# Optimization experiments

Measured on AMD Instinct MI355X. Metric: run time of the kernel, lower is better.

The kernel has to match this reference:

```python
import jax, jax.numpy as jnp
import numpy as np

D_MODEL = 2048
NUM_HEADS = 16
D_KV = D_MODEL // NUM_HEADS
THETA = 10000.0


def apply_rope(x, pos):
    # x: [B, H, S, d_kv], pos: [S] int
    d = x.shape[-1]
    inv_freq = 1.0 / (THETA ** (jnp.arange(0, d, 2, dtype=jnp.float32) / d))  # [d/2]
    ang = pos.astype(jnp.float32)[:, None] * inv_freq[None, :]  # [S, d/2]
    cos, sin = jnp.cos(ang), jnp.sin(ang)  # broadcast over B,H
    x1 = x[..., 0::2]
    x2 = x[..., 1::2]
    r1 = x1 * cos - x2 * sin
    r2 = x1 * sin + x2 * cos
    return jnp.stack([r1, r2], axis=-1).reshape(x.shape)


def setup_inputs() -> dict:
    key = jax.random.key(0)
    k = jax.random.split(key, 5)
    B, S = 2, 2048
    x = jax.random.normal(k[0], (B, S, D_MODEL), dtype=jnp.float32)
    scale = 1.0 / np.sqrt(D_MODEL)
    Wq = jax.random.normal(k[1], (D_MODEL, D_MODEL), dtype=jnp.float32) * scale
    Wk = jax.random.normal(k[2], (D_MODEL, D_MODEL), dtype=jnp.float32) * scale
    Wv = jax.random.normal(k[3], (D_MODEL, D_MODEL), dtype=jnp.float32) * scale
    Wo = jax.random.normal(k[4], (D_MODEL, D_MODEL), dtype=jnp.float32) * scale
    token_position = jnp.arange(S, dtype=jnp.int64 if jax.config.jax_enable_x64 else jnp.int32)
    return {"x": x, "Wq": Wq, "Wk": Wk, "Wv": Wv, "Wo": Wo, "token_position": token_position}


def reference(x, Wq, Wk, Wv, Wo, token_position):
    B, S, _ = x.shape
    def heads(y):
        return y.reshape(B, S, NUM_HEADS, D_KV).transpose(0, 2, 1, 3)  # [B,H,S,d]
    Q = heads(jnp.einsum('bsd,df->bsf', x, Wq))
    K = heads(jnp.einsum('bsd,df->bsf', x, Wk))
    V = heads(jnp.einsum('bsd,df->bsf', x, Wv))
    Q = apply_rope(Q, token_position)
    K = apply_rope(K, token_position)
    scale = 1.0 / jnp.sqrt(jnp.asarray(D_KV, dtype=x.dtype))
    scores = jnp.einsum('bhqd,bhkd->bhqk', Q, K) * scale  # [B,H,S,S]
    causal = jnp.tril(jnp.ones((S, S), dtype=bool))
    scores = jnp.where(causal, scores, -jnp.inf)
    attn = jax.nn.softmax(scores, axis=-1)
    out = jnp.einsum('bhqk,bhkd->bhqd', attn, V)  # [B,H,S,d]
    out = out.transpose(0, 2, 1, 3).reshape(B, S, D_MODEL)
    return jnp.einsum('bsd,df->bsf', out, Wo)
```

## Files before the change

kernel.cpp:

```cpp
#include <hip/hip_runtime.h>
#include <hip/hip_bf16.h>

#define S 2048
#define DM 2048
#define NH 16
#define DH 128

typedef __attribute__((ext_vector_type(8))) short short8;
typedef __attribute__((ext_vector_type(4))) float floatx4;
typedef unsigned short u16;
typedef unsigned int u32;

__device__ __forceinline__ u16 f2bf(float f) {
  union { float f; u32 u; } v; v.f = f;
  u32 r = v.u + 0x7fffu + ((v.u >> 16) & 1u);
  return (u16)(r >> 16);
}
__device__ __forceinline__ u32 pack2(float lo, float hi) {
  float2 f; f.x = lo; f.y = hi;
  __hip_bfloat162 h = __float22bfloat162_rn(f);
  union { __hip_bfloat162 h; u32 u; } c; c.h = h;
  return c.u;
}

__device__ __forceinline__ floatx4 mfma16(short8 a, short8 b, floatx4 c) {
  return __builtin_amdgcn_mfma_f32_16x16x32_bf16(a, b, c, 0, 0, 0);
}

__device__ __forceinline__ void async_cp16(const u16* g, u16* l) {
  __builtin_amdgcn_global_load_lds(
      (const __attribute__((address_space(1))) void*)g,
      (__attribute__((address_space(3))) void*)l, 16, 0, 0);
}

__global__ void conv_x_k(const float* __restrict__ x, u16* __restrict__ xb) {
  int gid = blockIdx.x * 256 + threadIdx.x;
  float4 v = ((const float4*)x)[gid];
  uint2 p; p.x = pack2(v.x, v.y); p.y = pack2(v.z, v.w);
  ((uint2*)xb)[gid] = p;
}

__global__ void conv_w_k(const float* __restrict__ W0, const float* __restrict__ W1,
                         const float* __restrict__ W2, const float* __restrict__ W3,
                         u16* __restrict__ out) {
  __shared__ float tile[32][33];
  const float* W = blockIdx.z == 0 ? W0 : blockIdx.z == 1 ? W1 : blockIdx.z == 2 ? W2 : W3;
  u16* O = out + (size_t)blockIdx.z * DM * DM;
  int tx = threadIdx.x & 31, ty = threadIdx.x >> 5;
  int k0 = blockIdx.y * 32, n0 = blockIdx.x * 32;
#pragma unroll
  for (int j = 0; j < 4; j++)
    tile[ty + j * 8][tx] = W[(size_t)(k0 + ty + j * 8) * DM + n0 + tx];
  __syncthreads();
#pragma unroll
  for (int j = 0; j < 4; j++)
    O[(size_t)(n0 + ty + j * 8) * DM + k0 + tx] = f2bf(tile[tx][ty + j * 8]);
}

#define BM 256
#define BN 128
#define BK 32
#define NT 64

#define BARRIER __builtin_amdgcn_s_barrier()
#define SB __builtin_amdgcn_sched_barrier(0)
#define LGKM0 asm volatile("s_waitcnt lgkmcnt(0)" ::: "memory")

#define STG_A(q, j, koff) \
  async_cp16(pAg + (size_t)(j) * 64 * DM + (koff), &As[q][soff + (j) * 2048])
#define STG_B(q, j, koff) \
  async_cp16(pBg + (size_t)(j) * 64 * DM + (koff), &Bs[q][soff + (j) * 2048])

#define PH0(p) { \
    a0 = *(const short8*)&As[p][arow + xk]; \
    a1 = *(const short8*)&As[p][arow + 512 + xk]; \
    a2 = *(const short8*)&As[p][arow + 1024 + xk]; \
    a3 = *(const short8*)&As[p][arow + 1536 + xk]; \
    a4 = *(const short8*)&As[p][arow + 2048 + xk]; \
    a5 = *(const short8*)&As[p][arow + 2560 + xk]; \
    a6 = *(const short8*)&As[p][arow + 3072 + xk]; \
    a7 = *(const short8*)&As[p][arow + 3584 + xk]; \
    b0 = *(const short8*)&Bs[p][brow + xk]; \
    b1 = *(const short8*)&Bs[p][brow + 512 + xk]; \
    b2 = *(const short8*)&Bs[p][brow + 1024 + xk]; \
    b3 = *(const short8*)&Bs[p][brow + 1536 + xk]; \
    BARRIER; LGKM0; SB; \
    __builtin_amdgcn_s_setprio(1); \
    acc[0][0] = mfma16(a0, b0, acc[0][0]); \
    acc[1][0] = mfma16(a1, b0, acc[1][0]); \
    acc[2][0] = mfma16(a2, b0, acc[2][0]); \
    acc[3][0] = mfma16(a3, b0, acc[3][0]); \
    acc[0][1] = mfma16(a0, b1, acc[0][1]); \
    acc[1][1] = mfma16(a1, b1, acc[1][1]); \
    acc[2][1] = mfma16(a2, b1, acc[2][1]); \
    acc[3][1] = mfma16(a3, b1, acc[3][1]); \
    acc[0][2] = mfma16(a0, b2, acc[0][2]); \
    acc[1][2] = mfma16(a1, b2, acc[1][2]); \
    acc[2][2] = mfma16(a2, b2, acc[2][2]); \
    acc[3][2] = mfma16(a3, b2, acc[3][2]); \
    acc[0][3] = mfma16(a0, b3, acc[0][3]); \
    acc[1][3] = mfma16(a1, b3, acc[1][3]); \
    acc[2][3] = mfma16(a2, b3, acc[2][3]); \
    acc[3][3] = mfma16(a3, b3, acc[3][3]); \
    __builtin_amdgcn_s_setprio(0); \
    BARRIER; }

#define PH1(p, koff2, PRE2, LAST) { \
    if (PRE2) { STG_B(p, 0, koff2); STG_B(p, 1, koff2); \
                STG_A(p, 0, koff2); STG_A(p, 1, koff2); \
                STG_A(p, 2, koff2); STG_A(p, 3, koff2); } \
    SB; \
    __builtin_amdgcn_s_setprio(1); \
    acc[4][0] = mfma16(a4, b0, acc[4][0]); \
    acc[5][0] = mfma16(a5, b0, acc[5][0]); \
    acc[6][0] = mfma16(a6, b0, acc[6][0]); \
    acc[7][0] = mfma16(a7, b0, acc[7][0]); \
    acc[4][1] = mfma16(a4, b1, acc[4][1]); \
    acc[5][1] = mfma16(a5, b1, acc[5][1]); \
    acc[6][1] = mfma16(a6, b1, acc[6][1]); \
    acc[7][1] = mfma16(a7, b1, acc[7][1]); \
    acc[4][2] = mfma16(a4, b2, acc[4][2]); \
    acc[5][2] = mfma16(a5, b2, acc[5][2]); \
    acc[6][2] = mfma16(a6, b2, acc[6][2]); \
    acc[7][2] = mfma16(a7, b2, acc[7][2]); \
    acc[4][3] = mfma16(a4, b3, acc[4][3]); \
    acc[5][3] = mfma16(a5, b3, acc[5][3]); \
    acc[6][3] = mfma16(a6, b3, acc[6][3]); \
    acc[7][3] = mfma16(a7, b3, acc[7][3]); \
    __builtin_amdgcn_s_setprio(0); SB; \
    if (!LAST) { \
      if (PRE2) { asm volatile("s_waitcnt vmcnt(6)" ::: "memory"); } \
      else      { asm volatile("s_waitcnt vmcnt(0)" ::: "memory"); } \
      BARRIER; SB; } }

__global__ __launch_bounds__(256, 2)
void gemm_k(const u16* __restrict__ A, const u16* __restrict__ Wt,
            u16* __restrict__ oQ, u16* __restrict__ oK, u16* __restrict__ oV,
            const int* __restrict__ tp)
{
  __shared__ u16 As[2][BM * BK];
  __shared__ u16 Bs[2][BN * BK];
  const int t = threadIdx.x;
  const int w = t >> 6, lane = t & 63;
  const int l16 = lane & 15, quad = lane >> 4;
  const int wr = w >> 1, wc = w & 1;
  const int m0 = blockIdx.y * BM, n0 = blockIdx.x * BN;
  const u16* Bt = Wt + (size_t)blockIdx.z * DM * DM;

  const int srow = t >> 2;
  const int sc = ((t & 3) ^ ((t >> 3) & 3)) * 8;
  const u16* pAg = A + (size_t)(m0 + srow) * DM + sc;
  const u16* pBg = Bt + (size_t)(n0 + srow) * DM + sc;
  const int soff = t * 8;

  const int arow = (wr * 128 + l16) * 32;
  const int brow = (wc * 64 + l16) * 32;
  const int xk = ((quad ^ ((l16 >> 1) & 3)) << 3);

  floatx4 acc[8][4] = {};
  short8 a0, a1, a2, a3, a4, a5, a6, a7, b0, b1, b2, b3;

  STG_B(0, 0, 0); STG_B(0, 1, 0);
  STG_A(0, 0, 0); STG_A(0, 1, 0); STG_A(0, 2, 0); STG_A(0, 3, 0);
  STG_B(1, 0, BK); STG_B(1, 1, BK);
  STG_A(1, 0, BK); STG_A(1, 1, BK); STG_A(1, 2, BK); STG_A(1, 3, BK);
  SB;
  asm volatile("s_waitcnt vmcnt(6)" ::: "memory");
  BARRIER; SB;

  for (int it = 0; it < 31; ++it) {
    const int kE = (2 * it + 2) * BK;
    const int kO = (2 * it + 3) * BK;
    PH0(0) PH1(0, kE, 1, 0)
    PH0(1) PH1(1, kO, 1, 0)
  }
  PH0(0) PH1(0, 0, 0, 0)
  PH0(1) PH1(1, 0, 0, 1)

  const int mwb = m0 + wr * 128;
  const int nwb = n0 + wc * 64;
  if ((int)blockIdx.z == 2) {
#pragma unroll
    for (int mi = 0; mi < 8; mi++) {
      int m = mwb + mi * 16 + quad * 4;
      int b = m >> 11, s = m & (S - 1);
#pragma unroll
      for (int ni = 0; ni < 4; ni++) {
        int f = nwb + ni * 16 + l16;
        int h = f >> 7, dh = f & (DH - 1);
        uint2 pk; pk.x = pack2(acc[mi][ni][0], acc[mi][ni][1]);
        pk.y = pack2(acc[mi][ni][2], acc[mi][ni][3]);
        *(uint2*)&oV[((size_t)(b * NH + h) * DH + dh) * S + s] = pk;
      }
    }
  } else {
    u16* Out = ((int)blockIdx.z == 0) ? oQ : oK;
    const float qs = ((int)blockIdx.z == 0) ? 0.12752780f : 1.0f;
#pragma unroll
    for (int mi = 0; mi < 8; mi++) {
#pragma unroll
      for (int r = 0; r < 4; r++) {
        int m = mwb + mi * 16 + quad * 4 + r;
        int b = m >> 11, s = m & (S - 1);
        int ps = tp[s];
#pragma unroll
        for (int ni = 0; ni < 4; ni++) {
          int f = nwb + ni * 16 + l16;
          int h = f >> 7, dh = f & (DH - 1);
          float own = acc[mi][ni][r];
          float oth = __shfl_xor(own, 1, 64);
          float fr = __expf((float)(dh & ~1) * (-9.210340371976184f / 128.0f));
          float ang = (float)ps * fr;
          float sn, cs; __sincosf(ang, &sn, &cs);
          float res = (dh & 1) ? (oth * sn + own * cs) : (own * cs - oth * sn);
          Out[((size_t)(b * NH + h) * S + s) * DH + dh] = f2bf(res * qs);
        }
      }
    }
  }
}

__global__ __launch_bounds__(256, 4)
void oproj_k(const u16* __restrict__ A, const u16* __restrict__ Wt,
             float* __restrict__ oO)
{
  __shared__ u16 As2[128 * 32];
  __shared__ u16 Bs2[128 * 32];
  const int t = threadIdx.x;
  const int w = t >> 6, lane = t & 63;
  const int l16 = lane & 15, quad = lane >> 4;
  const int m0 = blockIdx.y * 128, n0 = blockIdx.x * 128;
  const int wm = (w >> 1) * 64, wn = (w & 1) * 64;
  const u16* Bt = Wt + (size_t)3 * DM * DM;

  const u16* pA[2]; const u16* pB[2]; u16* lA[2]; u16* lB[2];
#pragma unroll
  for (int i = 0; i < 2; i++) {
    int unit = i * 256 + t;
    int row = unit >> 2, s = unit & 3;
    int c = s ^ ((row >> 1) & 3);
    pA[i] = A + (size_t)(m0 + row) * DM + c * 8;
    pB[i] = Bt + (size_t)(n0 + row) * DM + c * 8;
    lA[i] = &As2[unit * 8];
    lB[i] = &Bs2[unit * 8];
  }

  floatx4 acc[4][4] = {};

  for (int k0 = 0; k0 < DM; k0 += 32) {
#pragma unroll
    for (int i = 0; i < 2; i++) {
      async_cp16(pA[i] + k0, lA[i]);
      async_cp16(pB[i] + k0, lB[i]);
    }
    __syncthreads();
    short8 af[4], bfr[4];
#pragma unroll
    for (int i = 0; i < 4; i++) {
      int row = wm + i * 16 + l16;
      af[i] = *(short8*)&As2[(row * 4 + (quad ^ ((row >> 1) & 3))) * 8];
    }
#pragma unroll
    for (int i = 0; i < 4; i++) {
      int row = wn + i * 16 + l16;
      bfr[i] = *(short8*)&Bs2[(row * 4 + (quad ^ ((row >> 1) & 3))) * 8];
    }
#pragma unroll
    for (int mi = 0; mi < 4; mi++)
#pragma unroll
      for (int ni = 0; ni < 4; ni++)
        acc[mi][ni] = mfma16(af[mi], bfr[ni], acc[mi][ni]);
    __syncthreads();
  }

#pragma unroll
  for (int mi = 0; mi < 4; mi++) {
    int m = m0 + wm + mi * 16 + quad * 4;
#pragma unroll
    for (int ni = 0; ni < 4; ni++) {
      int n = n0 + wn + ni * 16 + l16;
#pragma unroll
      for (int r = 0; r < 4; r++)
        oO[(size_t)(m + r) * DM + n] = acc[mi][ni][r];
    }
  }
}

#define ATILE(p, i) { \
    const int k0a = (i) * 64; \
    floatx4 sc[4] = {}; \
    __builtin_amdgcn_s_setprio(1); \
    _Pragma("unroll") \
    for (int hh = 0; hh < 4; hh++) { \
      int row = hh * 16 + l16; \
      _Pragma("unroll") \
      for (int kc = 0; kc < 4; kc++) { \
        short8 kf = *(short8*)&Ks[p][row * 128 + (((kc * 4 + quad) ^ l16) << 3)]; \
        sc[hh] = mfma16(kf, aq[kc], sc[hh]); \
      } \
    } \
    __builtin_amdgcn_s_setprio(0); \
    if (k0a + 64 > qt) { \
      _Pragma("unroll") \
      for (int hh = 0; hh < 4; hh++) \
        _Pragma("unroll") \
        for (int r = 0; r < 4; r++) { \
          int j = k0a + hh * 16 + quad * 4 + r; \
          if (j > qt + l16) sc[hh][r] = -3.0e38f; \
        } \
    } \
    _Pragma("unroll") \
    for (int hh = 0; hh < 4; hh++) { \
      float e0 = __builtin_amdgcn_exp2f(fminf(sc[hh][0], 44.0f)); \
      float e1 = __builtin_amdgcn_exp2f(fminf(sc[hh][1], 44.0f)); \
      float e2 = __builtin_amdgcn_exp2f(fminf(sc[hh][2], 44.0f)); \
      float e3 = __builtin_amdgcn_exp2f(fminf(sc[hh][3], 44.0f)); \
      lsum += (e0 + e1) + (e2 + e3); \
      uint2 pk; pk.x = pack2(e0, e1); pk.y = pack2(e2, e3); \
      int su = (2 * hh + (quad >> 1)) ^ pxor; \
      *(uint2*)&Pw[l16 * 64 + su * 8 + (quad & 1) * 4] = pk; \
    } \
    LGKM0; SB; \
    BARRIER;                        \
    if ((i) + 2 < nt) { \
      _Pragma("unroll") \
      for (int j = 0; j < 4; j++) \
        async_cp16(pK[j] + (size_t)(k0a + 128) * DH, &Ks[p][lKo[j]]); \
    } \
    __builtin_amdgcn_s_setprio(1); \
    _Pragma("unroll") \
    for (int c = 0; c < 2; c++) { \
      short8 pf = *(short8*)&Pw[l16 * 64 + (((4 * c + quad) ^ pxor) << 3)]; \
      _Pragma("unroll") \
      for (int t8 = 0; t8 < 8; t8++) { \
        int row = t8 * 16 + l16; \
        short8 av = *(short8*)&Vs[p][row * 64 + (((c * 4 + quad) ^ (l16 & 7)) << 3)]; \
        o[t8] = mfma16(av, pf, o[t8]); \
      } \
    } \
    __builtin_amdgcn_s_setprio(0); \
    LGKM0; SB; \
    BARRIER;                        \
    if ((i) + 2 < nt) { \
      _Pragma("unroll") \
      for (int j = 0; j < 4; j++) \
        async_cp16(pV[j] + k0a + 128, &Vs[p][lVo[j]]); \
    } \
    if ((i) + 1 < nt) { \
      SB; \
      if ((i) + 2 < nt) { asm volatile("s_waitcnt vmcnt(8)" ::: "memory"); } \
      else              { asm volatile("s_waitcnt vmcnt(0)" ::: "memory"); } \
      BARRIER; SB; \
    } \
  }

__global__ __launch_bounds__(256, 2)
void attn_k(const u16* __restrict__ Q, const u16* __restrict__ K,
            const u16* __restrict__ Vt, u16* __restrict__ O)
{
  __shared__ u16 Ks[2][64 * 128];
  __shared__ u16 Vs[2][128 * 64];
  __shared__ u16 P[4][16 * 64];
  const int t = threadIdx.x, w = t >> 6, lane = t & 63;
  const int l16 = lane & 15, quad = lane >> 4;
  const int task = blockIdx.x;
  const int bh = task & 31, b = bh >> 4, h = bh & 15;
  const int g = 31 - (task >> 5);
  const int qg = g * 64;
  const int qt = qg + w * 16;
  const int nt = g + 1;
  const u16* Qb = Q + (size_t)bh * S * DH;
  const u16* Kb = K + (size_t)bh * S * DH;
  const u16* Vb = Vt + (size_t)bh * DH * S;
  u16* Pw = P[w];
  const int pxor = l16 & 7;

  const u16* pK[4]; int lKo[4];
  const u16* pV[4]; int lVo[4];
#pragma unroll
  for (int j = 0; j < 4; j++) {
    int kr = w * 16 + j * 4 + quad;
    int ks = l16;
    int kc = ks ^ (kr & 15);
    pK[j] = Kb + (size_t)kr * DH + kc * 8;
    lKo[j] = kr * 128 + ks * 8;
    int vr = w * 32 + j * 8 + (lane >> 3);
    int vs = lane & 7;
    int vc = vs ^ (vr & 7);
    pV[j] = Vb + (size_t)vr * S + vc * 8;
    lVo[j] = vr * 64 + vs * 8;
  }

  short8 aq[4];
#pragma unroll
  for (int kc = 0; kc < 4; kc++)
    aq[kc] = *(const short8*)&Qb[(size_t)(qt + l16) * DH + kc * 32 + quad * 8];

  floatx4 o[8] = {};
  float lsum = 0.0f;

#pragma unroll
  for (int j = 0; j < 4; j++) async_cp16(pK[j], &Ks[0][lKo[j]]);
#pragma unroll
  for (int j = 0; j < 4; j++) async_cp16(pV[j], &Vs[0][lVo[j]]);
  if (nt > 1) {
#pragma unroll
    for (int j = 0; j < 4; j++) async_cp16(pK[j] + (size_t)64 * DH, &Ks[1][lKo[j]]);
#pragma unroll
    for (int j = 0; j < 4; j++) async_cp16(pV[j] + 64, &Vs[1][lVo[j]]);
    SB;
    asm volatile("s_waitcnt vmcnt(8)" ::: "memory");
  } else {
    SB;
    asm volatile("s_waitcnt vmcnt(0)" ::: "memory");
  }
  BARRIER; SB;

  int i = 0;
  for (; i + 2 <= nt; i += 2) {
    ATILE(0, i)
    ATILE(1, i + 1)
  }
  if (i < nt) { ATILE(0, i) }

  float l = lsum + __shfl_xor(lsum, 16, 64);
  l += __shfl_xor(l, 32, 64);
  float inv = __builtin_amdgcn_rcpf(l);
#pragma unroll
  for (int t8 = 0; t8 < 8; t8++) {
    uint2 pa;
    pa.x = pack2(o[t8][0] * inv, o[t8][1] * inv);
    pa.y = pack2(o[t8][2] * inv, o[t8][3] * inv);
    *(uint2*)&O[((size_t)(b * S + qt + l16)) * DM + h * DH + t8 * 16 + quad * 4] = pa;
  }
}

extern "C" void kernel_launch(void* const* d_in, const int* in_sizes, int n_in,
                              void* d_out, int out_size, void* d_ws, size_t ws_size,
                              hipStream_t stream) {
  const float* x  = (const float*)d_in[0];
  const float* Wq = (const float*)d_in[1];
  const float* Wk = (const float*)d_in[2];
  const float* Wv = (const float*)d_in[3];
  const float* Wo = (const float*)d_in[4];
  const int*   tp = (const int*)d_in[5];

  char* ws = (char*)d_ws;
  u16* Wt = (u16*)ws;
  u16* xb = (u16*)(ws + 33554432);
  u16* Qb = (u16*)(ws + 50331648);
  u16* Kb = (u16*)(ws + 67108864);
  u16* Vb = (u16*)(ws + 83886080);
  u16* Ob = (u16*)(ws + 100663296);

  conv_x_k<<<8192, 256, 0, stream>>>(x, xb);
  conv_w_k<<<dim3(64, 64, 4), 256, 0, stream>>>(Wq, Wk, Wv, Wo, Wt);
  gemm_k<<<dim3(16, 16, 3), 256, 0, stream>>>(xb, Wt, Qb, Kb, Vb, tp);
  attn_k<<<1024, 256, 0, stream>>>(Qb, Kb, Vb, Ob);
  oproj_k<<<dim3(16, 32), 256, 0, stream>>>(Ob, Wt, (float*)d_out);
}
```

Measured before the change: 369.3 us.

## Double attention query tile per block to 128 rows, halving K/V loads

```diff
diff --git a/kernel.cpp b/kernel.cpp
--- a/kernel.cpp
+++ b/kernel.cpp
@@ -288,37 +288,44 @@
 
 #define ATILE(p, i) { \
     const int k0a = (i) * 64; \
-    floatx4 sc[4] = {}; \
-    __builtin_amdgcn_s_setprio(1); \
-    _Pragma("unroll") \
-    for (int hh = 0; hh < 4; hh++) { \
-      int row = hh * 16 + l16; \
+    if (k0a <= qt + 31) { \
       _Pragma("unroll") \
-      for (int kc = 0; kc < 4; kc++) { \
-        short8 kf = *(short8*)&Ks[p][row * 128 + (((kc * 4 + quad) ^ l16) << 3)]; \
-        sc[hh] = mfma16(kf, aq[kc], sc[hh]); \
+      for (int hh = 0; hh < 4; hh++) { \
+        int row = hh * 16 + l16; \
+        floatx4 s0 = {0.f, 0.f, 0.f, 0.f}; \
+        floatx4 s1 = {0.f, 0.f, 0.f, 0.f}; \
+        __builtin_amdgcn_s_setprio(1); \
+        _Pragma("unroll") \
+        for (int kc = 0; kc < 4; kc++) { \
+          short8 kf = *(short8*)&Ks[p][row * 128 + (((kc * 4 + quad) ^ l16) << 3)]; \
+          s0 = mfma16(kf, aq0[kc], s0); \
+          s1 = mfma16(kf, aq1[kc], s1); \
+        } \
+        __builtin_amdgcn_s_setprio(0); \
+        if (k0a + 64 > qt) { \
+          _Pragma("unroll") \
+          for (int r = 0; r < 4; r++) { \
+            int jj = k0a + hh * 16 + quad * 4 + r; \
+            if (jj > qt + l16) s0[r] = -3.0e38f; \
+            if (jj > qt + 16 + l16) s1[r] = -3.0e38f; \
+          } \
+        } \
+        int su = (2 * hh + (quad >> 1)) ^ pxor; \
+        float e0 = __builtin_amdgcn_exp2f(fminf(s0[0], 44.0f)); \
+        float e1 = __builtin_amdgcn_exp2f(fminf(s0[1], 44.0f)); \
+        float e2 = __builtin_amdgcn_exp2f(fminf(s0[2], 44.0f)); \
+        float e3 = __builtin_amdgcn_exp2f(fminf(s0[3], 44.0f)); \
+        lsum0 += (e0 + e1) + (e2 + e3); \
+        uint2 pk0; pk0.x = pack2(e0, e1); pk0.y = pack2(e2, e3); \
+        *(uint2*)&Pw[l16 * 64 + su * 8 + (quad & 1) * 4] = pk0; \
+        e0 = __builtin_amdgcn_exp2f(fminf(s1[0], 44.0f)); \
+        e1 = __builtin_amdgcn_exp2f(fminf(s1[1], 44.0f)); \
+        e2 = __builtin_amdgcn_exp2f(fminf(s1[2], 44.0f)); \
+        e3 = __builtin_amdgcn_exp2f(fminf(s1[3], 44.0f)); \
+        lsum1 += (e0 + e1) + (e2 + e3); \
+        uint2 pk1; pk1.x = pack2(e0, e1); pk1.y = pack2(e2, e3); \
+        *(uint2*)&Pw[(16 + l16) * 64 + su * 8 + (quad & 1) * 4] = pk1; \
       } \
-    } \
-    __builtin_amdgcn_s_setprio(0); \
-    if (k0a + 64 > qt) { \
-      _Pragma("unroll") \
-      for (int hh = 0; hh < 4; hh++) \
-        _Pragma("unroll") \
-        for (int r = 0; r < 4; r++) { \
-          int j = k0a + hh * 16 + quad * 4 + r; \
-          if (j > qt + l16) sc[hh][r] = -3.0e38f; \
-        } \
-    } \
-    _Pragma("unroll") \
-    for (int hh = 0; hh < 4; hh++) { \
-      float e0 = __builtin_amdgcn_exp2f(fminf(sc[hh][0], 44.0f)); \
-      float e1 = __builtin_amdgcn_exp2f(fminf(sc[hh][1], 44.0f)); \
-      float e2 = __builtin_amdgcn_exp2f(fminf(sc[hh][2], 44.0f)); \
-      float e3 = __builtin_amdgcn_exp2f(fminf(sc[hh][3], 44.0f)); \
-      lsum += (e0 + e1) + (e2 + e3); \
-      uint2 pk; pk.x = pack2(e0, e1); pk.y = pack2(e2, e3); \
-      int su = (2 * hh + (quad >> 1)) ^ pxor; \
-      *(uint2*)&Pw[l16 * 64 + su * 8 + (quad & 1) * 4] = pk; \
     } \
     LGKM0; SB; \
     BARRIER;                        \
@@ -327,18 +334,22 @@
       for (int j = 0; j < 4; j++) \
         async_cp16(pK[j] + (size_t)(k0a + 128) * DH, &Ks[p][lKo[j]]); \
     } \
-    __builtin_amdgcn_s_setprio(1); \
-    _Pragma("unroll") \
-    for (int c = 0; c < 2; c++) { \
-      short8 pf = *(short8*)&Pw[l16 * 64 + (((4 * c + quad) ^ pxor) << 3)]; \
+    if (k0a <= qt + 31) { \
+      __builtin_amdgcn_s_setprio(1); \
       _Pragma("unroll") \
-      for (int t8 = 0; t8 < 8; t8++) { \
-        int row = t8 * 16 + l16; \
-        short8 av = *(short8*)&Vs[p][row * 64 + (((c * 4 + quad) ^ (l16 & 7)) << 3)]; \
-        o[t8] = mfma16(av, pf, o[t8]); \
+      for (int c = 0; c < 2; c++) { \
+        short8 pf0 = *(short8*)&Pw[l16 * 64 + (((4 * c + quad) ^ pxor) << 3)]; \
+        short8 pf1 = *(short8*)&Pw[(16 + l16) * 64 + (((4 * c + quad) ^ pxor) << 3)]; \
+        _Pragma("unroll") \
+        for (int t8 = 0; t8 < 8; t8++) { \
+          int row = t8 * 16 + l16; \
+          short8 av = *(short8*)&Vs[p][row * 64 + (((c * 4 + quad) ^ (l16 & 7)) << 3)]; \
+          o0[t8] = mfma16(av, pf0, o0[t8]); \
+          o1[t8] = mfma16(av, pf1, o1[t8]); \
+        } \
       } \
+      __builtin_amdgcn_s_setprio(0); \
     } \
-    __builtin_amdgcn_s_setprio(0); \
     LGKM0; SB; \
     BARRIER;                        \
     if ((i) + 2 < nt) { \
@@ -360,15 +371,17 @@
 {
   __shared__ u16 Ks[2][64 * 128];
   __shared__ u16 Vs[2][128 * 64];
-  __shared__ u16 P[4][16 * 64];
+  __shared__ u16 P[4][32 * 64];
   const int t = threadIdx.x, w = t >> 6, lane = t & 63;
   const int l16 = lane & 15, quad = lane >> 4;
   const int task = blockIdx.x;
-  const int bh = task & 31, b = bh >> 4, h = bh & 15;
-  const int g = 31 - (task >> 5);
-  const int qg = g * 64;
-  const int qt = qg + w * 16;
-  const int nt = g + 1;
+  const int half = task >> 8, idx = task & 255;
+  const int slot = idx >> 5, bh = idx & 31;
+  const int b = bh >> 4, h = bh & 15;
+  const int gq = half ? slot : (15 - slot);
+  const int qg = gq * 128;
+  const int qt = qg + w * 32;
+  const int nt = 2 * gq + 2;
   const u16* Qb = Q + (size_t)bh * S * DH;
   const u16* Kb = K + (size_t)bh * S * DH;
   const u16* Vb = Vt + (size_t)bh * DH * S;
@@ -391,47 +404,48 @@
     lVo[j] = vr * 64 + vs * 8;
   }
 
-  short8 aq[4];
-#pragma unroll
-  for (int kc = 0; kc < 4; kc++)
-    aq[kc] = *(const short8*)&Qb[(size_t)(qt + l16) * DH + kc * 32 + quad * 8];
-
-  floatx4 o[8] = {};
-  float lsum = 0.0f;
+  short8 aq0[4], aq1[4];
+#pragma unroll
+  for (int kc = 0; kc < 4; kc++) {
+    aq0[kc] = *(const short8*)&Qb[(size_t)(qt + l16) * DH + kc * 32 + quad * 8];
+    aq1[kc] = *(const short8*)&Qb[(size_t)(qt + 16 + l16) * DH + kc * 32 + quad * 8];
+  }
+
+  floatx4 o0[8] = {}, o1[8] = {};
+  float lsum0 = 0.0f, lsum1 = 0.0f;
 
 #pragma unroll
   for (int j = 0; j < 4; j++) async_cp16(pK[j], &Ks[0][lKo[j]]);
 #pragma unroll
   for (int j = 0; j < 4; j++) async_cp16(pV[j], &Vs[0][lVo[j]]);
-  if (nt > 1) {
-#pragma unroll
-    for (int j = 0; j < 4; j++) async_cp16(pK[j] + (size_t)64 * DH, &Ks[1][lKo[j]]);
-#pragma unroll
-    for (int j = 0; j < 4; j++) async_cp16(pV[j] + 64, &Vs[1][lVo[j]]);
-    SB;
-    asm volatile("s_waitcnt vmcnt(8)" ::: "memory");
-  } else {
-    SB;
-    asm volatile("s_waitcnt vmcnt(0)" ::: "memory");
-  }
+#pragma unroll
+  for (int j = 0; j < 4; j++) async_cp16(pK[j] + (size_t)64 * DH, &Ks[1][lKo[j]]);
+#pragma unroll
+  for (int j = 0; j < 4; j++) async_cp16(pV[j] + 64, &Vs[1][lVo[j]]);
+  SB;
+  asm volatile("s_waitcnt vmcnt(8)" ::: "memory");
   BARRIER; SB;
 
-  int i = 0;
-  for (; i + 2 <= nt; i += 2) {
+  for (int i = 0; i < nt; i += 2) {
     ATILE(0, i)
     ATILE(1, i + 1)
   }
-  if (i < nt) { ATILE(0, i) }
-
-  float l = lsum + __shfl_xor(lsum, 16, 64);
-  l += __shfl_xor(l, 32, 64);
-  float inv = __builtin_amdgcn_rcpf(l);
+
+  float l0 = lsum0 + __shfl_xor(lsum0, 16, 64);
+  l0 += __shfl_xor(l0, 32, 64);
+  float l1 = lsum1 + __shfl_xor(lsum1, 16, 64);
+  l1 += __shfl_xor(l1, 32, 64);
+  float inv0 = __builtin_amdgcn_rcpf(l0);
+  float inv1 = __builtin_amdgcn_rcpf(l1);
 #pragma unroll
   for (int t8 = 0; t8 < 8; t8++) {
     uint2 pa;
-    pa.x = pack2(o[t8][0] * inv, o[t8][1] * inv);
-    pa.y = pack2(o[t8][2] * inv, o[t8][3] * inv);
+    pa.x = pack2(o0[t8][0] * inv0, o0[t8][1] * inv0);
+    pa.y = pack2(o0[t8][2] * inv0, o0[t8][3] * inv0);
     *(uint2*)&O[((size_t)(b * S + qt + l16)) * DM + h * DH + t8 * 16 + quad * 4] = pa;
+    pa.x = pack2(o1[t8][0] * inv1, o1[t8][1] * inv1);
+    pa.y = pack2(o1[t8][2] * inv1, o1[t8][3] * inv1);
+    *(uint2*)&O[((size_t)(b * S + qt + 16 + l16)) * DM + h * DH + t8 * 16 + quad * 4] = pa;
   }
 }
 
@@ -456,6 +470,6 @@
   conv_x_k<<<8192, 256, 0, stream>>>(x, xb);
   conv_w_k<<<dim3(64, 64, 4), 256, 0, stream>>>(Wq, Wk, Wv, Wo, Wt);
   gemm_k<<<dim3(16, 16, 3), 256, 0, stream>>>(xb, Wt, Qb, Kb, Vb, tp);
-  attn_k<<<1024, 256, 0, stream>>>(Qb, Kb, Vb, Ob);
+  attn_k<<<512, 256, 0, stream>>>(Qb, Kb, Vb, Ob);
   oproj_k<<<dim3(16, 32), 256, 0, stream>>>(Ob, Wt, (float*)d_out);
 }
```

Measured after the change: 386.2 us. +4.6%, slower.
